# Performance work log

Hardware: AMD Instinct MI355X
Metric: run time of the kernel (lower is better)

The kernel has to match this reference:

```python
import jax, jax.numpy as jnp
import numpy as np

NUM_HEADING_BIN = 12
NUM_SIZE_CLUSTER = 8
DELTA_NORM_W = 0.01
CENTER_W = 0.5
B, N = 4096, 2048


def huber(err, delta=1.0):
    a = jnp.abs(err)
    q = jnp.minimum(a, delta)
    return jnp.mean(0.5 * q * q + delta * (a - q))


def box3d_corners(centers, headings, sizes):
    # centers (B,3), headings (B,), sizes (B,3) -> (B,8,3)
    l, w, h = sizes[:, 0:1], sizes[:, 1:2], sizes[:, 2:3]
    sx = jnp.asarray([1, 1, -1, -1, 1, 1, -1, -1], dtype=sizes.dtype)
    sy = jnp.asarray([1, -1, -1, 1, 1, -1, -1, 1], dtype=sizes.dtype)
    sz = jnp.asarray([1, 1, 1, 1, -1, -1, -1, -1], dtype=sizes.dtype)
    corners = jnp.stack([0.5 * l * sx, 0.5 * w * sy, 0.5 * h * sz], axis=1)  # (B,3,8)
    c, s = jnp.cos(headings), jnp.sin(headings)
    z, o = jnp.zeros_like(c), jnp.ones_like(c)
    R = jnp.stack([jnp.stack([c, -s, z], -1),
                   jnp.stack([s, c, z], -1),
                   jnp.stack([z, z, o], -1)], axis=1)  # (B,3,3)
    out = jnp.einsum('bij,bjk->bik', R, corners) + centers[:, :, None]
    return jnp.transpose(out, (0, 2, 1))  # (B,8,3)


def setup_inputs() -> dict:
    key = jax.random.key(0)
    ks = jax.random.split(key, 9)
    return {
        'mask_xyz_mean': jax.random.normal(ks[0], (B, 3), jnp.float32),
        'point_cloud': jax.random.normal(ks[1], (B, 3, N), jnp.float32),
        'x_delta': jax.random.normal(ks[2], (B, 3, N), jnp.float32),
        'center_label': jax.random.normal(ks[3], (B, 3), jnp.float32),
        'size_residual_label': jax.random.normal(ks[4], (B, 3), jnp.float32),
        'heading_residual_label': jax.random.normal(ks[5], (B,), jnp.float32),
        'mean_sizes': jax.random.uniform(ks[6], (NUM_SIZE_CLUSTER, 3), jnp.float32, 0.5, 2.5),
        'size_class_label': jax.random.randint(ks[7], (B,), 0, NUM_SIZE_CLUSTER, jnp.int32),
        'heading_class_label': jax.random.randint(ks[8], (B,), 0, NUM_HEADING_BIN, jnp.int32),
    }


def reference(mask_xyz_mean, point_cloud, x_delta, center_label,
              size_residual_label, heading_residual_label, mean_sizes,
              size_class_label, heading_class_label):
    eps = 0.0  # faithful: original has no eps
    # center loss
    center_dist = jnp.linalg.norm(mask_xyz_mean - center_label, axis=1)
    center_loss = CENTER_W * huber(center_dist)

    # label assembly (onehot-sum == gather)
    size_label = mean_sizes[size_class_label] + size_residual_label  # (B,3)
    bin_centers = jnp.arange(0, np.pi, np.pi / NUM_HEADING_BIN, dtype=jnp.float32)
    heading_label = heading_residual_label + bin_centers[heading_class_label]  # (B,)

    corners_3d_gt = box3d_corners(center_label, heading_label, size_label)
    corners_2d_gt = corners_3d_gt[:, 4:8, :2]  # (B,4,2)

    v = center_label[:, :2]  # (B,2)
    p_dir = jnp.stack([-v[:, 1], v[:, 0]], axis=1)
    p_dir = p_dir / jnp.linalg.norm(p_dir, axis=1, keepdims=True)  # (B,2)

    pp_label = jnp.einsum('bkc,bc->bk', corners_2d_gt, p_dir)  # (B,4)
    py_max, py_min = jnp.max(pp_label, axis=1), jnp.min(pp_label, axis=1)
    std_y_label = (py_max - py_min) / 4
    mean_y_label = (py_max + py_min) / 2

    v_norm = jnp.linalg.norm(v, axis=1, keepdims=True)  # (B,1)
    proj_label = jnp.einsum('bkc,bc->bk', corners_2d_gt, v) / v_norm  # (B,4)
    p_max, p_min = jnp.max(proj_label, axis=1), jnp.min(proj_label, axis=1)
    std_label = (p_max - p_min) / 4
    mean_label = (p_max + p_min) / 2

    pc_xy = jnp.transpose(point_cloud, (0, 2, 1))[:, :, :2]  # (B,N,2)

    pp_pc = jnp.einsum('bnc,bc->bn', pc_xy, p_dir)  # (B,N)
    std_y_pc = jnp.std(pp_pc, axis=1, ddof=1)
    mean_y_pc = jnp.mean(pp_pc, axis=1)
    y_std_loss = huber(jnp.abs(std_y_label - std_y_pc))
    y_mean_loss = huber(jnp.abs(mean_y_label - mean_y_pc))

    proj_pc = jnp.einsum('bnc,bc->bn', pc_xy, v) / v_norm  # (B,N)
    std_pc = jnp.std(proj_pc, axis=1, ddof=1)
    mean_pc = jnp.mean(proj_pc, axis=1)
    x_std_loss = huber(jnp.abs(std_label - std_pc))
    x_mean_loss = huber(jnp.abs(mean_label - mean_pc))

    delta_norm = jnp.sqrt(jnp.sum(x_delta * x_delta, axis=(1, 2)))
    delta_norm_loss = DELTA_NORM_W * huber(delta_norm)

    total = center_loss + x_std_loss + x_mean_loss + delta_norm_loss + y_mean_loss + y_std_loss
    return 0.4 * total
```

## Files before the change

### kernel.cpp

```cpp
#include <hip/hip_runtime.h>
#include <math.h>

#define B_SZ 4096
#define N_PTS 2048
#define BLOCK 256
#define SWEEP_BLOCKS 2048
#define XD_ITERS 12
#define PC_ITERS 4

#define WS_PC  0
#define WS_XD  131072
#define WS_TOT (131072 + 98304)

__device__ __forceinline__ float huber1(float a) {
    float q = fminf(a, 1.0f);
    return 0.5f * q * q + (a - q);
}

__global__ __launch_bounds__(BLOCK, 8) void sweep(
    const float* __restrict__ point_cloud,
    const float* __restrict__ x_delta,
    const float* __restrict__ center_label,
    float* __restrict__ ws)
{
    const int tid  = threadIdx.x;
    const int wave = tid >> 6;
    const int lane = tid & 63;

    if (blockIdx.x < SWEEP_BLOCKS) {
        const int s = blockIdx.x;
        const float4* xd4 = (const float4*)x_delta;
        float* __restrict__ wxd = ws + WS_XD;
        #pragma unroll
        for (int k = 0; k < XD_ITERS; ++k) {
            const int W = s + k * SWEEP_BLOCKS;
            const float4 d = xd4[(size_t)W * 256 + tid];
            float v = d.x * d.x + d.y * d.y + d.z * d.z + d.w * d.w;
            #pragma unroll
            for (int off = 32; off > 0; off >>= 1)
                v += __shfl_down(v, off, 64);
            if (lane == 0) wxd[W * 4 + wave] = v;
        }
    } else {
        const int s = blockIdx.x - SWEEP_BLOCKS;
        const float4* pc4 = (const float4*)point_cloud;
        float4* __restrict__ wpc = (float4*)(ws + WS_PC);
        #pragma unroll
        for (int k = 0; k < PC_ITERS; ++k) {
            const int W = s + k * SWEEP_BLOCKS;
            const int e = W >> 1;
            const int h = W & 1;
            const float cx = center_label[e * 3 + 0];
            const float cy = center_label[e * 3 + 1];
            const float vn  = sqrtf(cx * cx + cy * cy);
            const float pdx = -cy / vn;
            const float pdy =  cx / vn;

            const size_t fx = (size_t)e * 1536 + h * 256 + tid;
            const float4 x4 = pc4[fx];
            const float4 y4 = pc4[fx + 512];

            float s_pp = 0.f, s_pp2 = 0.f, s_t = 0.f, s_t2 = 0.f;
            {
                const float xs[4] = {x4.x, x4.y, x4.z, x4.w};
                const float ys[4] = {y4.x, y4.y, y4.z, y4.w};
                #pragma unroll
                for (int j = 0; j < 4; ++j) {
                    const float pp = xs[j] * pdx + ys[j] * pdy;
                    const float t  = xs[j] * cx  + ys[j] * cy;
                    s_pp += pp; s_pp2 += pp * pp; s_t += t; s_t2 += t * t;
                }
            }
            #pragma unroll
            for (int off = 32; off > 0; off >>= 1) {
                s_pp  += __shfl_down(s_pp,  off, 64);
                s_pp2 += __shfl_down(s_pp2, off, 64);
                s_t   += __shfl_down(s_t,   off, 64);
                s_t2  += __shfl_down(s_t2,  off, 64);
            }
            if (lane == 0)
                wpc[W * 4 + wave] = make_float4(s_pp, s_pp2, s_t, s_t2);
        }
    }
}

__global__ __launch_bounds__(BLOCK) void finalize(
    const float* __restrict__ mask_xyz_mean,
    const float* __restrict__ center_label,
    const float* __restrict__ size_residual,
    const float* __restrict__ heading_residual,
    const float* __restrict__ mean_sizes,
    const int*   __restrict__ size_class,
    const int*   __restrict__ heading_class,
    float* __restrict__ ws)
{
    const int e = blockIdx.x * BLOCK + threadIdx.x;

    float s_pp = 0.f, s_pp2 = 0.f, s_t = 0.f, s_t2 = 0.f;
    const float4* pcp = ((const float4*)(ws + WS_PC)) + (size_t)e * 8;
    #pragma unroll
    for (int i = 0; i < 8; ++i) {
        const float4 p = pcp[i];
        s_pp += p.x; s_pp2 += p.y; s_t += p.z; s_t2 += p.w;
    }
    float s_d2 = 0.f;
    const float4* xdp = ((const float4*)(ws + WS_XD)) + (size_t)e * 6;
    #pragma unroll
    for (int i = 0; i < 6; ++i) {
        const float4 p = xdp[i];
        s_d2 += (p.x + p.y) + (p.z + p.w);
    }

    const float cx = center_label[e * 3 + 0];
    const float cy = center_label[e * 3 + 1];
    const float cz = center_label[e * 3 + 2];
    const float vnorm2 = cx * cx + cy * cy;
    const float vnorm  = sqrtf(vnorm2);
    const float pdx = -cy / vnorm;
    const float pdy =  cx / vnorm;

    const float mx = mask_xyz_mean[e * 3 + 0];
    const float my = mask_xyz_mean[e * 3 + 1];
    const float mz = mask_xyz_mean[e * 3 + 2];
    const float dxc = mx - cx, dyc = my - cy, dzc = mz - cz;
    const float center_dist = sqrtf(dxc * dxc + dyc * dyc + dzc * dzc);

    const int sc = size_class[e];
    const float l  = mean_sizes[sc * 3 + 0] + size_residual[e * 3 + 0];
    const float w_ = mean_sizes[sc * 3 + 1] + size_residual[e * 3 + 1];

    const float theta = heading_residual[e] +
                        (float)heading_class[e] * (float)(M_PI / 12.0);
    const float c = cosf(theta);
    const float s = sinf(theta);
    const float hl = 0.5f * l, hw = 0.5f * w_;

    float X[4], Y[4];
    X[0] =  c * hl - s * hw + cx;  Y[0] =  s * hl + c * hw + cy;
    X[1] =  c * hl + s * hw + cx;  Y[1] =  s * hl - c * hw + cy;
    X[2] = -c * hl + s * hw + cx;  Y[2] = -s * hl - c * hw + cy;
    X[3] = -c * hl - s * hw + cx;  Y[3] = -s * hl + c * hw + cy;

    float ppmax = -INFINITY, ppmin = INFINITY;
    float pmax  = -INFINITY, pmin  = INFINITY;
    #pragma unroll
    for (int k = 0; k < 4; ++k) {
        const float pp = X[k] * pdx + Y[k] * pdy;
        const float pj = (X[k] * cx + Y[k] * cy) / vnorm;
        ppmax = fmaxf(ppmax, pp); ppmin = fminf(ppmin, pp);
        pmax  = fmaxf(pmax,  pj); pmin  = fminf(pmin,  pj);
    }
    const float std_y_label  = (ppmax - ppmin) * 0.25f;
    const float mean_y_label = (ppmax + ppmin) * 0.5f;
    const float std_label    = (pmax - pmin) * 0.25f;
    const float mean_label   = (pmax + pmin) * 0.5f;

    const float invN   = 1.0f / (float)N_PTS;
    const float invNm1 = 1.0f / (float)(N_PTS - 1);

    const float mean_y_pc = s_pp * invN;
    const float var_y = (s_pp2 - s_pp * s_pp * invN) * invNm1;
    const float std_y_pc = sqrtf(fmaxf(var_y, 0.0f));

    const float mean_pc = (s_t * invN) / vnorm;
    const float var_x = ((s_t2 - s_t * s_t * invN) * invNm1) / vnorm2;
    const float std_pc = sqrtf(fmaxf(var_x, 0.0f));

    const float delta_norm = sqrtf(s_d2);

    const float total =
          0.5f  * huber1(center_dist)
        +         huber1(fabsf(std_label  - std_pc))
        +         huber1(fabsf(mean_label - mean_pc))
        + 0.01f * huber1(delta_norm)
        +         huber1(fabsf(mean_y_label - mean_y_pc))
        +         huber1(fabsf(std_y_label  - std_y_pc));

    ws[WS_TOT + e] = total;
}

__global__ __launch_bounds__(BLOCK) void loss_reduce(
    const float* __restrict__ ws, float* __restrict__ out)
{
    const int tid = threadIdx.x;
    const float4* w4 = (const float4*)(ws + WS_TOT);

    float s = 0.f;
    #pragma unroll
    for (int k = 0; k < B_SZ / 4 / BLOCK; ++k) {
        const float4 v = w4[tid + k * BLOCK];
        s += v.x + v.y + v.z + v.w;
    }

    #pragma unroll
    for (int off = 32; off > 0; off >>= 1)
        s += __shfl_down(s, off, 64);

    __shared__ float red[BLOCK / 64];
    const int wave = tid >> 6;
    const int lane = tid & 63;
    if (lane == 0) red[wave] = s;
    __syncthreads();

    if (tid == 0) {
        #pragma unroll
        for (int w = 1; w < BLOCK / 64; ++w) s += red[w];
        out[0] = s * (0.4f / (float)B_SZ);
    }
}

extern "C" void kernel_launch(void* const* d_in, const int* in_sizes, int n_in,
                              void* d_out, int out_size, void* d_ws, size_t ws_size,
                              hipStream_t stream) {
    const float* mask_xyz_mean    = (const float*)d_in[0];
    const float* point_cloud      = (const float*)d_in[1];
    const float* x_delta          = (const float*)d_in[2];
    const float* center_label     = (const float*)d_in[3];
    const float* size_residual    = (const float*)d_in[4];
    const float* heading_residual = (const float*)d_in[5];
    const float* mean_sizes       = (const float*)d_in[6];
    const int*   size_class       = (const int*)d_in[7];
    const int*   heading_class    = (const int*)d_in[8];
    float* ws  = (float*)d_ws;
    float* out = (float*)d_out;

    sweep<<<2 * SWEEP_BLOCKS, BLOCK, 0, stream>>>(
        point_cloud, x_delta, center_label, ws);
    finalize<<<B_SZ / BLOCK, BLOCK, 0, stream>>>(
        mask_xyz_mean, center_label, size_residual, heading_residual,
        mean_sizes, size_class, heading_class, ws);
    loss_reduce<<<1, BLOCK, 0, stream>>>(ws, out);
}
```

Measured before the change: 223.8 us.

## Assign whole elements per block in sweep and use nontemporal loads

The sweep kernel's work split changes so each block processes two full batch elements instead of interleaved slices. Each thread issues several independent vector loads before reducing, and all streaming loads use nontemporal hints. This cuts per-element partial sums (4 per element instead of 8 or 24), shrinking the workspace written by sweep and read by finalize. The aim is more memory-level parallelism and less cache pollution on a bandwidth-bound sweep, at the cost of higher register use per thread.

```diff
diff --git a/kernel.cpp b/kernel.cpp
--- a/kernel.cpp
+++ b/kernel.cpp
@@ -4,13 +4,12 @@
 #define B_SZ 4096
 #define N_PTS 2048
 #define BLOCK 256
-#define SWEEP_BLOCKS 2048
-#define XD_ITERS 12
-#define PC_ITERS 4
-
-#define WS_PC  0
-#define WS_XD  131072
-#define WS_TOT (131072 + 98304)
+
+typedef float f4 __attribute__((ext_vector_type(4)));
+
+#define WS_PC   0
+#define WS_XD   65536
+#define WS_TOT  (65536 + 16384)
 
 __device__ __forceinline__ float huber1(float a) {
     float q = fminf(a, 1.0f);
@@ -27,45 +26,59 @@
     const int wave = tid >> 6;
     const int lane = tid & 63;
 
-    if (blockIdx.x < SWEEP_BLOCKS) {
+    if (blockIdx.x < (B_SZ / 2)) {
         const int s = blockIdx.x;
-        const float4* xd4 = (const float4*)x_delta;
-        float* __restrict__ wxd = ws + WS_XD;
+        const f4* xd4 = (const f4*)x_delta;
         #pragma unroll
-        for (int k = 0; k < XD_ITERS; ++k) {
-            const int W = s + k * SWEEP_BLOCKS;
-            const float4 d = xd4[(size_t)W * 256 + tid];
-            float v = d.x * d.x + d.y * d.y + d.z * d.z + d.w * d.w;
+        for (int e2 = 0; e2 < 2; ++e2) {
+            const int e = 2 * s + e2;
+            const f4* p = xd4 + (size_t)e * 1536;
+            const f4 d0 = __builtin_nontemporal_load(p + 0 * BLOCK + tid);
+            const f4 d1 = __builtin_nontemporal_load(p + 1 * BLOCK + tid);
+            const f4 d2 = __builtin_nontemporal_load(p + 2 * BLOCK + tid);
+            const f4 d3 = __builtin_nontemporal_load(p + 3 * BLOCK + tid);
+            const f4 d4 = __builtin_nontemporal_load(p + 4 * BLOCK + tid);
+            const f4 d5 = __builtin_nontemporal_load(p + 5 * BLOCK + tid);
+
+            float v = 0.f;
+            v += d0[0]*d0[0] + d0[1]*d0[1] + d0[2]*d0[2] + d0[3]*d0[3];
+            v += d1[0]*d1[0] + d1[1]*d1[1] + d1[2]*d1[2] + d1[3]*d1[3];
+            v += d2[0]*d2[0] + d2[1]*d2[1] + d2[2]*d2[2] + d2[3]*d2[3];
+            v += d3[0]*d3[0] + d3[1]*d3[1] + d3[2]*d3[2] + d3[3]*d3[3];
+            v += d4[0]*d4[0] + d4[1]*d4[1] + d4[2]*d4[2] + d4[3]*d4[3];
+            v += d5[0]*d5[0] + d5[1]*d5[1] + d5[2]*d5[2] + d5[3]*d5[3];
+
             #pragma unroll
             for (int off = 32; off > 0; off >>= 1)
                 v += __shfl_down(v, off, 64);
-            if (lane == 0) wxd[W * 4 + wave] = v;
+            if (lane == 0) ws[WS_XD + e * 4 + wave] = v;
         }
     } else {
-        const int s = blockIdx.x - SWEEP_BLOCKS;
-        const float4* pc4 = (const float4*)point_cloud;
-        float4* __restrict__ wpc = (float4*)(ws + WS_PC);
+        const int s = blockIdx.x - (B_SZ / 2);
+        const f4* pc4 = (const f4*)point_cloud;
+        f4* __restrict__ wpc = (f4*)(ws + WS_PC);
         #pragma unroll
-        for (int k = 0; k < PC_ITERS; ++k) {
-            const int W = s + k * SWEEP_BLOCKS;
-            const int e = W >> 1;
-            const int h = W & 1;
+        for (int e2 = 0; e2 < 2; ++e2) {
+            const int e = 2 * s + e2;
             const float cx = center_label[e * 3 + 0];
             const float cy = center_label[e * 3 + 1];
             const float vn  = sqrtf(cx * cx + cy * cy);
             const float pdx = -cy / vn;
             const float pdy =  cx / vn;
 
-            const size_t fx = (size_t)e * 1536 + h * 256 + tid;
-            const float4 x4 = pc4[fx];
-            const float4 y4 = pc4[fx + 512];
+            const f4* px = pc4 + (size_t)e * 1536;
+            const f4* py = px + 512;
+            const f4 x0 = __builtin_nontemporal_load(px + tid);
+            const f4 x1 = __builtin_nontemporal_load(px + BLOCK + tid);
+            const f4 y0 = __builtin_nontemporal_load(py + tid);
+            const f4 y1 = __builtin_nontemporal_load(py + BLOCK + tid);
 
             float s_pp = 0.f, s_pp2 = 0.f, s_t = 0.f, s_t2 = 0.f;
             {
-                const float xs[4] = {x4.x, x4.y, x4.z, x4.w};
-                const float ys[4] = {y4.x, y4.y, y4.z, y4.w};
+                const float xs[8] = {x0[0], x0[1], x0[2], x0[3], x1[0], x1[1], x1[2], x1[3]};
+                const float ys[8] = {y0[0], y0[1], y0[2], y0[3], y1[0], y1[1], y1[2], y1[3]};
                 #pragma unroll
-                for (int j = 0; j < 4; ++j) {
+                for (int j = 0; j < 8; ++j) {
                     const float pp = xs[j] * pdx + ys[j] * pdy;
                     const float t  = xs[j] * cx  + ys[j] * cy;
                     s_pp += pp; s_pp2 += pp * pp; s_t += t; s_t2 += t * t;
@@ -78,8 +91,10 @@
                 s_t   += __shfl_down(s_t,   off, 64);
                 s_t2  += __shfl_down(s_t2,  off, 64);
             }
-            if (lane == 0)
-                wpc[W * 4 + wave] = make_float4(s_pp, s_pp2, s_t, s_t2);
+            if (lane == 0) {
+                f4 r; r[0] = s_pp; r[1] = s_pp2; r[2] = s_t; r[3] = s_t2;
+                wpc[e * 4 + wave] = r;
+            }
         }
     }
 }
@@ -97,19 +112,15 @@
     const int e = blockIdx.x * BLOCK + threadIdx.x;
 
     float s_pp = 0.f, s_pp2 = 0.f, s_t = 0.f, s_t2 = 0.f;
-    const float4* pcp = ((const float4*)(ws + WS_PC)) + (size_t)e * 8;
-    #pragma unroll
-    for (int i = 0; i < 8; ++i) {
-        const float4 p = pcp[i];
-        s_pp += p.x; s_pp2 += p.y; s_t += p.z; s_t2 += p.w;
+    const f4* pcp = ((const f4*)(ws + WS_PC)) + (size_t)e * 4;
+    #pragma unroll
+    for (int i = 0; i < 4; ++i) {
+        const f4 p = pcp[i];
+        s_pp += p[0]; s_pp2 += p[1]; s_t += p[2]; s_t2 += p[3];
     }
     float s_d2 = 0.f;
-    const float4* xdp = ((const float4*)(ws + WS_XD)) + (size_t)e * 6;
-    #pragma unroll
-    for (int i = 0; i < 6; ++i) {
-        const float4 p = xdp[i];
-        s_d2 += (p.x + p.y) + (p.z + p.w);
-    }
+    #pragma unroll
+    for (int i = 0; i < 4; ++i) s_d2 += ws[WS_XD + e * 4 + i];
 
     const float cx = center_label[e * 3 + 0];
     const float cy = center_label[e * 3 + 1];
@@ -224,8 +235,7 @@
     float* ws  = (float*)d_ws;
     float* out = (float*)d_out;
 
-    sweep<<<2 * SWEEP_BLOCKS, BLOCK, 0, stream>>>(
-        point_cloud, x_delta, center_label, ws);
+    sweep<<<B_SZ, BLOCK, 0, stream>>>(point_cloud, x_delta, center_label, ws);
     finalize<<<B_SZ / BLOCK, BLOCK, 0, stream>>>(
         mask_xyz_mean, center_label, size_residual, heading_residual,
         mean_sizes, size_class, heading_class, ws);
```

Measured after the change: 207.1 us. 7.5% less time.
